# Performance work log

Hardware: AMD Instinct MI355X
Metric: run time of the kernel (lower is better)

## Reference

```python
import jax, jax.numpy as jnp
import numpy as np

T, E, B, D, N = 4, 4096, 2, 128, 384


def setup_inputs() -> dict:
    key = jax.random.key(0)
    ks = jax.random.split(key, 8)
    x = jax.random.normal(ks[0], (T, E, B, D), jnp.float32)
    feats = jax.random.normal(ks[1], (N, N, B, D), jnp.float32)
    # Node ids in [1, N]; id 0 is the padding row/col of the (N+1,N+1) grid.
    # Shared edge list across the batch (matches the repo's usage: the torch
    # scatter broadcasts one value over all batch slots, which is only
    # self-consistent when nodes are identical across batch).
    nodes1 = jax.random.randint(ks[2], (1, E, 2), 1, N + 1)
    nodes = jnp.broadcast_to(nodes1, (B, E, 2)).astype(jnp.int32)
    padding_mask = jnp.zeros((B, E), bool)
    padding_mask_feats = jnp.zeros((B, N), bool)
    pad = jax.random.normal(ks[3], (1,), jnp.float32)
    s1 = 1.0 / np.sqrt(D)
    s2 = 1.0 / np.sqrt(2 * D)
    W_g = jax.random.normal(ks[4], (D, D), jnp.float32) * s1
    b_g = jnp.zeros((D,), jnp.float32)
    W_lin = jax.random.normal(ks[5], (D, 2 * D), jnp.float32) * s2
    b_lin = jnp.zeros((D,), jnp.float32)
    W_f = jax.random.normal(ks[6], (D, D), jnp.float32) * s1
    b_f = jnp.zeros((D,), jnp.float32)
    return dict(x=x, feats=feats, nodes=nodes, padding_mask=padding_mask,
                padding_mask_feats=padding_mask_feats, pad=pad,
                W_g=W_g, b_g=b_g, W_lin=W_lin, b_lin=b_lin, W_f=W_f, b_f=b_f)


def _forward(x, feats, nodes, pad, W_g, b_g, W_lin, b_lin, W_f, b_f):
    # graph_layer stand-in: dense projection over embed dim
    x = jnp.einsum('tebd,od->tebo', x, W_g) + b_g            # (T,E,B,D)
    n_nodes, _, bsz, dim = feats.shape
    xmean = x.mean(0)                                        # (E,B,D)
    # dense padded (N+1,N+1,B,D) grid filled with learned pad value (faithful)
    grid = jnp.ones((n_nodes + 1, n_nodes + 1, bsz, dim), x.dtype) * pad
    n0 = nodes[0, :, 0]                                      # (E,) shared graph
    n1 = nodes[0, :, 1]
    grid = grid.at[n0, n1].set(xmean)                        # scatter edges into grid
    feats_update = grid[1:, 1:]                              # drop pad row/col -> (N,N,B,D)
    cat = jnp.concatenate([feats, feats_update], axis=-1)    # (N,N,B,2D)
    feats = jnp.einsum('nmbc,oc->nmbo', cat, W_lin) + b_lin  # Linear(2D -> D)
    # feat_layer stand-in: dense projection
    feats = jnp.einsum('nmbd,od->nmbo', feats, W_f) + b_f
    nodes_0 = jnp.maximum(nodes - 1, 0)                      # clamp after -1 shift
    g0 = nodes_0[:, :, 0].T                                  # (E,B)
    g1 = nodes_0[:, :, 1].T
    bidx = jnp.arange(bsz)[None, :]                          # (1,B)
    feats_subset = feats[g0, g1, bidx]                       # gather -> (E,B,D)
    x = x + feats_subset[None]                               # broadcast over trials
    return x, feats


def reference(x, feats, nodes, padding_mask, padding_mask_feats, pad,
              W_g, b_g, W_lin, b_lin, W_f, b_f):
    # padding masks are accepted for signature parity; the stub sub-layers
    # (single linear projections) do not consume them.
    return _forward(x, feats, nodes, pad, W_g, b_g, W_lin, b_lin, W_f, b_f)
```

## Files before the change

kernel.cpp:

```cpp
#include <hip/hip_runtime.h>
#include <hip/hip_bf16.h>


constexpr int T_ = 4, E_ = 4096, B_ = 2, D_ = 128, N_ = 384;
constexpr int EB = E_ * B_;
constexpr int XROWS = T_ * EB;
constexpr int NROWS = N_ * N_ * B_;
constexpr int NCELLS = N_ * N_;

typedef __attribute__((ext_vector_type(8))) short bf16x8;
typedef __attribute__((ext_vector_type(4))) float f32x4;
union BF8 { bf16x8 v; ushort u[8]; };

constexpr size_t OFF_WTG    = 0;
constexpr size_t OFF_WTL    = 16384;
constexpr size_t OFF_WTR    = 32768;
constexpr size_t OFF_BCOMB  = 49152;
constexpr size_t OFF_BP     = 49280;
constexpr size_t OFF_XMEAN  = 49408;
constexpr size_t OFF_UC     = OFF_XMEAN + (size_t)EB * D_;
constexpr size_t OFF_WIN    = OFF_UC + (size_t)EB * D_;
constexpr size_t OFF_BPACK  = OFF_WIN + (size_t)NCELLS;
constexpr size_t OFF_BPACKG = OFF_BPACK + 16384;
constexpr size_t OFF_BPACKR = OFF_BPACKG + 16384;
constexpr size_t WS_FLOATS  = OFF_BPACKR + 16384;

static __device__ inline ushort f2bf(float x) {
  const uint u = __float_as_uint(x);
  return (ushort)((u + 0x7fffu + ((u >> 16) & 1u)) >> 16);
}
static __device__ inline float bf2f(ushort h) {
  return __uint_as_float(((uint)h) << 16);
}

__global__ __launch_bounds__(256) void prep_kernel(
    const float* __restrict__ W_f, const float* __restrict__ W_lin,
    const float* __restrict__ W_g, const float* __restrict__ b_lin,
    const float* __restrict__ b_f, const float* __restrict__ pad,
    float* __restrict__ WtG, float* __restrict__ WtL, float* __restrict__ WtR,
    float* __restrict__ bcomb, float* __restrict__ bp, int* __restrict__ winner) {
  const int o = blockIdx.x;
  const int c = threadIdx.x;

  for (int i = blockIdx.x * 256 + c; i < NCELLS; i += 128 * 256) winner[i] = -1;

  float acc = 0.f;
#pragma unroll 4
  for (int d = 0; d < D_; ++d) acc += W_f[o * D_ + d] * W_lin[d * (2 * D_) + c];

  if (c < D_) {
    WtL[c * D_ + o] = acc;
    WtG[c * D_ + o] = W_g[o * D_ + c];
  } else {
    WtR[(c - D_) * D_ + o] = acc;
  }

  __shared__ float red[256];
  red[c] = (c >= D_) ? acc : 0.f;
  __syncthreads();
  for (int s = 128; s > 0; s >>= 1) {
    if (c < s) red[c] += red[c + s];
    __syncthreads();
  }
  const float padsum = red[0];
  __syncthreads();
  red[c] = (c < D_) ? W_f[o * D_ + c] * b_lin[c] : 0.f;
  __syncthreads();
  for (int s = 128; s > 0; s >>= 1) {
    if (c < s) red[c] += red[c + s];
    __syncthreads();
  }
  if (c == 0) {
    const float bc = b_f[o] + red[0];
    bcomb[o] = bc;
    bp[o] = bc + pad[0] * padsum;
  }
}

__global__ __launch_bounds__(64) void prep2_kernel(
    const float* __restrict__ Wkn, ushort* __restrict__ Bpack) {
  const int fi = blockIdx.x;
  const int l = threadIdx.x;
  const int ishi = (fi >> 5) ^ 1;
  const int k0 = (fi >> 3) & 3;
  const int n0 = fi & 7;
  const int o = n0 * 16 + (l & 15);
  const int kb = k0 * 32 + ((l >> 4) & 3) * 8;
  ushort* dst = Bpack + ((size_t)fi * 64 + l) * 8;
#pragma unroll
  for (int j = 0; j < 8; ++j) {
    const float w = Wkn[(size_t)(kb + j) * D_ + o];
    const ushort h = f2bf(w);
    if (ishi) {
      dst[j] = h;
    } else {
      dst[j] = f2bf(w - bf2f(h));
    }
  }
}

__global__ __launch_bounds__(256) void scatter_kernel(
    const int* __restrict__ nodes, int* __restrict__ winner) {
  const int e = blockIdx.x * 256 + threadIdx.x;
  if (e < E_) {
    const int n0 = nodes[e * 2 + 0];
    const int n1 = nodes[e * 2 + 1];
    atomicMax(&winner[(n0 - 1) * N_ + (n1 - 1)], e);
  }
}

__global__ __launch_bounds__(256) void tile_mfma_kernel(
    const float* __restrict__ A, const ushort* __restrict__ Bpack,
    const float* __restrict__ bias, float* __restrict__ out) {
  __shared__ float lw[64 * 128];
  const int tid = threadIdx.x;
  const size_t tile0 = (size_t)blockIdx.x * 64;

#pragma unroll
  for (int j = 0; j < 8; ++j) {
    const int idx = j * 256 + tid;
    const int row = idx >> 5;
    const int c4 = idx & 31;
    const float4 v = *(const float4*)&A[(tile0 + row) * D_ + c4 * 4];
    const int fidx = (row * 128 + c4 * 4) ^ ((row & 7) << 2);
    *(float4*)&lw[fidx] = v;
  }
  __syncthreads();

  const int wave = tid >> 6, lane = tid & 63;
  const int l15 = lane & 15;
  const int lh = (lane >> 4) & 3;
  const int arow = wave * 16 + l15;
  const int asw = (arow & 7) << 2;

  f32x4 acc[8];
#pragma unroll
  for (int n0 = 0; n0 < 8; ++n0) {
    const float b = bias ? bias[n0 * 16 + l15] : 0.f;
    acc[n0][0] = b; acc[n0][1] = b; acc[n0][2] = b; acc[n0][3] = b;
  }

  const bf16x8* __restrict__ bp8 = (const bf16x8*)Bpack;
#pragma unroll
  for (int k0 = 0; k0 < 4; ++k0) {
    const int base = arow * 128 + lh * 8 + k0 * 32;
    const float4 a0 = *(const float4*)&lw[(base + 0) ^ asw];
    const float4 a1 = *(const float4*)&lw[(base + 4) ^ asw];
    const float xs[8] = {a0.x, a0.y, a0.z, a0.w, a1.x, a1.y, a1.z, a1.w};
    BF8 ah, al;
#pragma unroll
    for (int j = 0; j < 8; ++j) {
      const ushort h = f2bf(xs[j]);
      ah.u[j] = h;
      al.u[j] = f2bf(xs[j] - bf2f(h));
    }
    bf16x8 bh[8];
#pragma unroll
    for (int n0 = 0; n0 < 8; ++n0)
      bh[n0] = bp8[(size_t)((0 * 32 + k0 * 8 + n0) * 64 + lane)];
#pragma unroll
    for (int n0 = 0; n0 < 8; ++n0) {
      acc[n0] = __builtin_amdgcn_mfma_f32_16x16x32_bf16(ah.v, bh[n0], acc[n0], 0, 0, 0);
      acc[n0] = __builtin_amdgcn_mfma_f32_16x16x32_bf16(al.v, bh[n0], acc[n0], 0, 0, 0);
    }
    bf16x8 bl[8];
#pragma unroll
    for (int n0 = 0; n0 < 8; ++n0)
      bl[n0] = bp8[(size_t)((1 * 32 + k0 * 8 + n0) * 64 + lane)];
#pragma unroll
    for (int n0 = 0; n0 < 8; ++n0)
      acc[n0] = __builtin_amdgcn_mfma_f32_16x16x32_bf16(ah.v, bl[n0], acc[n0], 0, 0, 0);
  }

  __syncthreads();
#pragma unroll
  for (int n0 = 0; n0 < 8; ++n0) {
    const int col = n0 * 16 + l15;
#pragma unroll
    for (int i = 0; i < 4; ++i) {
      const int row = wave * 16 + lh * 4 + i;
      lw[(row * 128 + col) ^ ((row & 7) << 2)] = acc[n0][i];
    }
  }
  __syncthreads();
#pragma unroll
  for (int j = 0; j < 8; ++j) {
    const int idx = j * 256 + tid;
    const int row = idx >> 5;
    const int c4 = idx & 31;
    const float4 v = *(const float4*)&lw[(row * 128 + c4 * 4) ^ ((row & 7) << 2)];
    *(float4*)&out[(tile0 + row) * D_ + c4 * 4] = v;
  }
}

__global__ __launch_bounds__(256) void mean_kernel(
    const float* __restrict__ out_x, float* __restrict__ xmean) {
  const int idx = blockIdx.x * 256 + threadIdx.x;
  const int pair = idx >> 5;
  const int o4 = (idx & 31) * 4;
  const size_t base = (size_t)pair * D_ + o4;
  float4 s = *(const float4*)&out_x[base];
  const float4 v1 = *(const float4*)&out_x[base + (size_t)1 * EB * D_];
  const float4 v2 = *(const float4*)&out_x[base + (size_t)2 * EB * D_];
  const float4 v3 = *(const float4*)&out_x[base + (size_t)3 * EB * D_];
  s.x = (s.x + v1.x + v2.x + v3.x) * 0.25f;
  s.y = (s.y + v1.y + v2.y + v3.y) * 0.25f;
  s.z = (s.z + v1.z + v2.z + v3.z) * 0.25f;
  s.w = (s.w + v1.w + v2.w + v3.w) * 0.25f;
  *(float4*)&xmean[base] = s;
}

__global__ __launch_bounds__(256) void fixup_kernel(
    const int* __restrict__ nodes, const int* __restrict__ winner,
    const float* __restrict__ uc, const float* __restrict__ bcomb,
    const float* __restrict__ bp, float* __restrict__ out_feats) {
  const int e = blockIdx.x;
  const int n0 = nodes[e * 2 + 0] - 1;
  const int n1 = nodes[e * 2 + 1] - 1;
  const int cell = n0 * N_ + n1;
  if (winner[cell] != e) return;
  const int t = threadIdx.x;
  const int b = t >> 7, o = t & 127;
  out_feats[((size_t)cell * 2 + b) * D_ + o] +=
      uc[((size_t)e * 2 + b) * D_ + o] + bcomb[o] - bp[o];
}

__global__ __launch_bounds__(256) void gather_add_kernel(
    const int* __restrict__ nodes, const float* __restrict__ out_feats,
    float* __restrict__ out_x) {
  const int e = blockIdx.x;
  const int tid = threadIdx.x;
  const int b = tid >> 7, o = tid & 127;
  const int n0 = nodes[((size_t)b * E_ + e) * 2 + 0] - 1;
  const int n1 = nodes[((size_t)b * E_ + e) * 2 + 1] - 1;
  const float fs = out_feats[(((size_t)n0 * N_ + n1) * B_ + b) * D_ + o];
#pragma unroll
  for (int t = 0; t < T_; ++t)
    out_x[(((size_t)t * E_ + e) * B_ + b) * D_ + o] += fs;
}

extern "C" void kernel_launch(void* const* d_in, const int* in_sizes, int n_in,
                              void* d_out, int out_size, void* d_ws, size_t ws_size,
                              hipStream_t stream) {
  const float* x      = (const float*)d_in[0];
  const float* feats  = (const float*)d_in[1];
  const int*   nodes  = (const int*)d_in[2];
  const float* pad    = (const float*)d_in[5];
  const float* W_g    = (const float*)d_in[6];
  const float* b_g    = (const float*)d_in[7];
  const float* W_lin  = (const float*)d_in[8];
  const float* b_lin  = (const float*)d_in[9];
  const float* W_f    = (const float*)d_in[10];
  const float* b_f    = (const float*)d_in[11];

  float* out_x     = (float*)d_out;
  float* out_feats = out_x + (size_t)T_ * E_ * B_ * D_;

  if (ws_size < WS_FLOATS * sizeof(float) + 16) return;

  float*  wsf    = (float*)d_ws;
  float*  WtG    = wsf + OFF_WTG;
  float*  WtL    = wsf + OFF_WTL;
  float*  WtR    = wsf + OFF_WTR;
  float*  bcomb  = wsf + OFF_BCOMB;
  float*  bpv    = wsf + OFF_BP;
  float*  xmean  = wsf + OFF_XMEAN;
  float*  uc     = wsf + OFF_UC;
  int*    win    = (int*)(wsf + OFF_WIN);
  ushort* Bpack  = (ushort*)(wsf + OFF_BPACK);
  ushort* BpackG = (ushort*)(wsf + OFF_BPACKG);
  ushort* BpackR = (ushort*)(wsf + OFF_BPACKR);

  prep_kernel<<<dim3(128), dim3(256), 0, stream>>>(W_f, W_lin, W_g, b_lin, b_f,
                                                   pad, WtG, WtL, WtR, bcomb,
                                                   bpv, win);
  prep2_kernel<<<dim3(64), dim3(64), 0, stream>>>(WtL, Bpack);
  prep2_kernel<<<dim3(64), dim3(64), 0, stream>>>(WtG, BpackG);
  prep2_kernel<<<dim3(64), dim3(64), 0, stream>>>(WtR, BpackR);
  scatter_kernel<<<dim3(E_ / 256), dim3(256), 0, stream>>>(nodes, win);

  tile_mfma_kernel<<<dim3(XROWS / 64), dim3(256), 0, stream>>>(x, BpackG, b_g,
                                                               out_x);
  mean_kernel<<<dim3(EB * 32 / 256), dim3(256), 0, stream>>>(out_x, xmean);
  tile_mfma_kernel<<<dim3(EB / 64), dim3(256), 0, stream>>>(xmean, BpackR,
                                                            nullptr, uc);
  tile_mfma_kernel<<<dim3(NROWS / 64), dim3(256), 0, stream>>>(feats, Bpack,
                                                               bpv, out_feats);
  fixup_kernel<<<dim3(E_), dim3(256), 0, stream>>>(nodes, win, uc, bcomb, bpv,
                                                   out_feats);
  gather_add_kernel<<<dim3(E_), dim3(256), 0, stream>>>(nodes, out_feats,
                                                        out_x);
}
```

Baseline: 400.8 us.

## Make tile GEMM persistent with prefetch, cache B in LDS, fold W_g into mean path

The tile MFMA kernel becomes a persistent grid-stride loop. It prefetches the next A tile into registers while computing the current one, and stages the high-bf16 B fragments in shared memory. The mean-over-trials projection now uses a precomposed weight (W_lin right half times W_g) with a folded bias. The mean is computed directly from the input x, which removes the dependency on the first GEMM's output. This reduces memory latency stalls and launch/tail overhead, at the cost of more registers and LDS per block and a small extra prep kernel.

```diff
diff --git a/kernel.cpp b/kernel.cpp
--- a/kernel.cpp
+++ b/kernel.cpp
@@ -4,6 +4,7 @@
 
 constexpr int T_ = 4, E_ = 4096, B_ = 2, D_ = 128, N_ = 384;
 constexpr int EB = E_ * B_;
+constexpr int XSTRIDE_T = E_ * B_ * D_;
 constexpr int XROWS = T_ * EB;
 constexpr int NROWS = N_ * N_ * B_;
 constexpr int NCELLS = N_ * N_;
@@ -23,7 +24,9 @@
 constexpr size_t OFF_BPACK  = OFF_WIN + (size_t)NCELLS;
 constexpr size_t OFF_BPACKG = OFF_BPACK + 16384;
 constexpr size_t OFF_BPACKR = OFF_BPACKG + 16384;
-constexpr size_t WS_FLOATS  = OFF_BPACKR + 16384;
+constexpr size_t OFF_WGR    = OFF_BPACKR + 16384;
+constexpr size_t OFF_BGR    = OFF_WGR + 16384;
+constexpr size_t WS_FLOATS  = OFF_BGR + 128;
 
 static __device__ inline ushort f2bf(float x) {
   const uint u = __float_as_uint(x);
@@ -75,6 +78,27 @@
     bcomb[o] = bc;
     bp[o] = bc + pad[0] * padsum;
   }
+}
+
+__global__ __launch_bounds__(128) void prepB_kernel(
+    const float* __restrict__ WtR, const float* __restrict__ W_g,
+    const float* __restrict__ b_g, float* __restrict__ Wgr_kn,
+    float* __restrict__ bgr) {
+  const int o = blockIdx.x;
+  const int c = threadIdx.x;
+  float acc = 0.f;
+#pragma unroll 4
+  for (int d = 0; d < D_; ++d) acc += WtR[d * D_ + o] * W_g[d * D_ + c];
+  Wgr_kn[c * D_ + o] = acc;
+
+  __shared__ float red[128];
+  red[c] = WtR[c * D_ + o] * b_g[c];
+  __syncthreads();
+  for (int s = 64; s > 0; s >>= 1) {
+    if (c < s) red[c] += red[c + s];
+    __syncthreads();
+  }
+  if (c == 0) bgr[o] = red[0];
 }
 
 __global__ __launch_bounds__(64) void prep2_kernel(
@@ -111,98 +135,130 @@
 
 __global__ __launch_bounds__(256) void tile_mfma_kernel(
     const float* __restrict__ A, const ushort* __restrict__ Bpack,
-    const float* __restrict__ bias, float* __restrict__ out) {
-  __shared__ float lw[64 * 128];
+    const float* __restrict__ bias, float* __restrict__ out, int ntiles) {
+  __shared__ float lA[64 * 128];
+  __shared__ bf16x8 lBhi[2048];
   const int tid = threadIdx.x;
-  const size_t tile0 = (size_t)blockIdx.x * 64;
-
-#pragma unroll
-  for (int j = 0; j < 8; ++j) {
-    const int idx = j * 256 + tid;
-    const int row = idx >> 5;
-    const int c4 = idx & 31;
-    const float4 v = *(const float4*)&A[(tile0 + row) * D_ + c4 * 4];
-    const int fidx = (row * 128 + c4 * 4) ^ ((row & 7) << 2);
-    *(float4*)&lw[fidx] = v;
-  }
-  __syncthreads();
+  const int stride = gridDim.x;
+
+  {
+    const bf16x8* src = (const bf16x8*)Bpack;
+    for (int i = tid; i < 2048; i += 256) lBhi[i] = src[i];
+  }
 
   const int wave = tid >> 6, lane = tid & 63;
   const int l15 = lane & 15;
   const int lh = (lane >> 4) & 3;
   const int arow = wave * 16 + l15;
   const int asw = (arow & 7) << 2;
-
-  f32x4 acc[8];
-#pragma unroll
-  for (int n0 = 0; n0 < 8; ++n0) {
-    const float b = bias ? bias[n0 * 16 + l15] : 0.f;
-    acc[n0][0] = b; acc[n0][1] = b; acc[n0][2] = b; acc[n0][3] = b;
-  }
-
   const bf16x8* __restrict__ bp8 = (const bf16x8*)Bpack;
-#pragma unroll
-  for (int k0 = 0; k0 < 4; ++k0) {
-    const int base = arow * 128 + lh * 8 + k0 * 32;
-    const float4 a0 = *(const float4*)&lw[(base + 0) ^ asw];
-    const float4 a1 = *(const float4*)&lw[(base + 4) ^ asw];
-    const float xs[8] = {a0.x, a0.y, a0.z, a0.w, a1.x, a1.y, a1.z, a1.w};
-    BF8 ah, al;
+
+  float bs8[8];
+#pragma unroll
+  for (int n0 = 0; n0 < 8; ++n0) bs8[n0] = bias ? bias[n0 * 16 + l15] : 0.f;
+
+  int tile = blockIdx.x;
+  float4 pf[8];
+  if (tile < ntiles) {
+    const size_t t0 = (size_t)tile * 64;
 #pragma unroll
     for (int j = 0; j < 8; ++j) {
-      const ushort h = f2bf(xs[j]);
-      ah.u[j] = h;
-      al.u[j] = f2bf(xs[j] - bf2f(h));
-    }
-    bf16x8 bh[8];
-#pragma unroll
-    for (int n0 = 0; n0 < 8; ++n0)
-      bh[n0] = bp8[(size_t)((0 * 32 + k0 * 8 + n0) * 64 + lane)];
+      const int idx = j * 256 + tid;
+      pf[j] = *(const float4*)&A[(t0 + (idx >> 5)) * D_ + (idx & 31) * 4];
+    }
+  }
+
+  for (; tile < ntiles; tile += stride) {
+    const size_t tile0 = (size_t)tile * 64;
+    __syncthreads();
+#pragma unroll
+    for (int j = 0; j < 8; ++j) {
+      const int idx = j * 256 + tid;
+      const int row = idx >> 5, c4 = idx & 31;
+      *(float4*)&lA[(row * 128 + c4 * 4) ^ ((row & 7) << 2)] = pf[j];
+    }
+    __syncthreads();
+
+    const int next = tile + stride;
+    if (next < ntiles) {
+      const size_t t0 = (size_t)next * 64;
+#pragma unroll
+      for (int j = 0; j < 8; ++j) {
+        const int idx = j * 256 + tid;
+        pf[j] = *(const float4*)&A[(t0 + (idx >> 5)) * D_ + (idx & 31) * 4];
+      }
+    }
+
+    f32x4 acc[8];
 #pragma unroll
     for (int n0 = 0; n0 < 8; ++n0) {
-      acc[n0] = __builtin_amdgcn_mfma_f32_16x16x32_bf16(ah.v, bh[n0], acc[n0], 0, 0, 0);
-      acc[n0] = __builtin_amdgcn_mfma_f32_16x16x32_bf16(al.v, bh[n0], acc[n0], 0, 0, 0);
-    }
-    bf16x8 bl[8];
-#pragma unroll
-    for (int n0 = 0; n0 < 8; ++n0)
-      bl[n0] = bp8[(size_t)((1 * 32 + k0 * 8 + n0) * 64 + lane)];
-#pragma unroll
-    for (int n0 = 0; n0 < 8; ++n0)
-      acc[n0] = __builtin_amdgcn_mfma_f32_16x16x32_bf16(ah.v, bl[n0], acc[n0], 0, 0, 0);
-  }
-
-  __syncthreads();
-#pragma unroll
-  for (int n0 = 0; n0 < 8; ++n0) {
-    const int col = n0 * 16 + l15;
-#pragma unroll
-    for (int i = 0; i < 4; ++i) {
-      const int row = wave * 16 + lh * 4 + i;
-      lw[(row * 128 + col) ^ ((row & 7) << 2)] = acc[n0][i];
-    }
-  }
-  __syncthreads();
-#pragma unroll
-  for (int j = 0; j < 8; ++j) {
-    const int idx = j * 256 + tid;
-    const int row = idx >> 5;
-    const int c4 = idx & 31;
-    const float4 v = *(const float4*)&lw[(row * 128 + c4 * 4) ^ ((row & 7) << 2)];
-    *(float4*)&out[(tile0 + row) * D_ + c4 * 4] = v;
+      acc[n0][0] = bs8[n0]; acc[n0][1] = bs8[n0];
+      acc[n0][2] = bs8[n0]; acc[n0][3] = bs8[n0];
+    }
+
+#pragma unroll
+    for (int k0 = 0; k0 < 4; ++k0) {
+      bf16x8 bl[8];
+#pragma unroll
+      for (int n0 = 0; n0 < 8; ++n0)
+        bl[n0] = bp8[(size_t)((32 + k0 * 8 + n0) * 64 + lane)];
+      const int base = arow * 128 + lh * 8 + k0 * 32;
+      const float4 a0 = *(const float4*)&lA[(base + 0) ^ asw];
+      const float4 a1 = *(const float4*)&lA[(base + 4) ^ asw];
+      const float xs[8] = {a0.x, a0.y, a0.z, a0.w, a1.x, a1.y, a1.z, a1.w};
+      BF8 ah, al;
+#pragma unroll
+      for (int j = 0; j < 8; ++j) {
+        const ushort h = f2bf(xs[j]);
+        ah.u[j] = h;
+        al.u[j] = f2bf(xs[j] - bf2f(h));
+      }
+      bf16x8 bh[8];
+#pragma unroll
+      for (int n0 = 0; n0 < 8; ++n0)
+        bh[n0] = lBhi[(k0 * 8 + n0) * 64 + lane];
+#pragma unroll
+      for (int n0 = 0; n0 < 8; ++n0) {
+        acc[n0] = __builtin_amdgcn_mfma_f32_16x16x32_bf16(ah.v, bh[n0], acc[n0], 0, 0, 0);
+        acc[n0] = __builtin_amdgcn_mfma_f32_16x16x32_bf16(al.v, bh[n0], acc[n0], 0, 0, 0);
+      }
+#pragma unroll
+      for (int n0 = 0; n0 < 8; ++n0)
+        acc[n0] = __builtin_amdgcn_mfma_f32_16x16x32_bf16(ah.v, bl[n0], acc[n0], 0, 0, 0);
+    }
+
+    __syncthreads();
+#pragma unroll
+    for (int n0 = 0; n0 < 8; ++n0) {
+      const int col = n0 * 16 + l15;
+#pragma unroll
+      for (int i = 0; i < 4; ++i) {
+        const int row = wave * 16 + lh * 4 + i;
+        lA[(row * 128 + col) ^ ((row & 7) << 2)] = acc[n0][i];
+      }
+    }
+    __syncthreads();
+#pragma unroll
+    for (int j = 0; j < 8; ++j) {
+      const int idx = j * 256 + tid;
+      const int row = idx >> 5, c4 = idx & 31;
+      const float4 v =
+          *(const float4*)&lA[(row * 128 + c4 * 4) ^ ((row & 7) << 2)];
+      *(float4*)&out[(tile0 + row) * D_ + c4 * 4] = v;
+    }
   }
 }
 
 __global__ __launch_bounds__(256) void mean_kernel(
-    const float* __restrict__ out_x, float* __restrict__ xmean) {
+    const float* __restrict__ x, float* __restrict__ xmean) {
   const int idx = blockIdx.x * 256 + threadIdx.x;
   const int pair = idx >> 5;
   const int o4 = (idx & 31) * 4;
   const size_t base = (size_t)pair * D_ + o4;
-  float4 s = *(const float4*)&out_x[base];
-  const float4 v1 = *(const float4*)&out_x[base + (size_t)1 * EB * D_];
-  const float4 v2 = *(const float4*)&out_x[base + (size_t)2 * EB * D_];
-  const float4 v3 = *(const float4*)&out_x[base + (size_t)3 * EB * D_];
+  float4 s = *(const float4*)&x[base];
+  const float4 v1 = *(const float4*)&x[base + (size_t)1 * XSTRIDE_T];
+  const float4 v2 = *(const float4*)&x[base + (size_t)2 * XSTRIDE_T];
+  const float4 v3 = *(const float4*)&x[base + (size_t)3 * XSTRIDE_T];
   s.x = (s.x + v1.x + v2.x + v3.x) * 0.25f;
   s.y = (s.y + v1.y + v2.y + v3.y) * 0.25f;
   s.z = (s.z + v1.z + v2.z + v3.z) * 0.25f;
@@ -270,22 +326,25 @@
   ushort* Bpack  = (ushort*)(wsf + OFF_BPACK);
   ushort* BpackG = (ushort*)(wsf + OFF_BPACKG);
   ushort* BpackR = (ushort*)(wsf + OFF_BPACKR);
+  float*  WgrKn  = wsf + OFF_WGR;
+  float*  bgr    = wsf + OFF_BGR;
 
   prep_kernel<<<dim3(128), dim3(256), 0, stream>>>(W_f, W_lin, W_g, b_lin, b_f,
                                                    pad, WtG, WtL, WtR, bcomb,
                                                    bpv, win);
+  prepB_kernel<<<dim3(128), dim3(128), 0, stream>>>(WtR, W_g, b_g, WgrKn, bgr);
   prep2_kernel<<<dim3(64), dim3(64), 0, stream>>>(WtL, Bpack);
   prep2_kernel<<<dim3(64), dim3(64), 0, stream>>>(WtG, BpackG);
-  prep2_kernel<<<dim3(64), dim3(64), 0, stream>>>(WtR, BpackR);
+  prep2_kernel<<<dim3(64), dim3(64), 0, stream>>>(WgrKn, BpackR);
   scatter_kernel<<<dim3(E_ / 256), dim3(256), 0, stream>>>(nodes, win);
-
-  tile_mfma_kernel<<<dim3(XROWS / 64), dim3(256), 0, stream>>>(x, BpackG, b_g,
-                                                               out_x);
-  mean_kernel<<<dim3(EB * 32 / 256), dim3(256), 0, stream>>>(out_x, xmean);
-  tile_mfma_kernel<<<dim3(EB / 64), dim3(256), 0, stream>>>(xmean, BpackR,
-                                                            nullptr, uc);
-  tile_mfma_kernel<<<dim3(NROWS / 64), dim3(256), 0, stream>>>(feats, Bpack,
-                                                               bpv, out_feats);
+  mean_kernel<<<dim3(EB * 32 / 256), dim3(256), 0, stream>>>(x, xmean);
+
+  tile_mfma_kernel<<<dim3(512), dim3(256), 0, stream>>>(x, BpackG, b_g, out_x,
+                                                        XROWS / 64);
+  tile_mfma_kernel<<<dim3(128), dim3(256), 0, stream>>>(xmean, BpackR, bgr, uc,
+                                                        EB / 64);
+  tile_mfma_kernel<<<dim3(512), dim3(256), 0, stream>>>(feats, Bpack, bpv,
+                                                        out_feats, NROWS / 64);
   fixup_kernel<<<dim3(E_), dim3(256), 0, stream>>>(nodes, win, uc, bcomb, bpv,
                                                    out_feats);
   gather_add_kernel<<<dim3(E_), dim3(256), 0, stream>>>(nodes, out_feats,
```

New measurement: 482.6 us. +20.4%, slower.
